# Kernel tuning notes

Measured on AMD Instinct MI355X. Metric: run time of the kernel, lower is better.

Reference implementation:

```python
import jax, jax.numpy as jnp
import numpy as np

D_MODEL = 128
D_STATE = 64
EXPAND = 2
D_INNER = EXPAND * D_MODEL  # 256
D_CONV = 4
DT_RANK = (D_MODEL + 15) // 16  # 8
EPS = 1e-6


def setup_inputs() -> dict:
    key = jax.random.key(0)
    ks = jax.random.split(key, 10)
    B, L = 8, 4096
    s = lambda *sh: 1.0 / np.sqrt(sh[-1])
    inp = {
        "x": jax.random.normal(ks[0], (B, L, D_MODEL), jnp.float32),
        "norm_w": jnp.ones((D_MODEL,), jnp.float32),
        "norm_b": jnp.zeros((D_MODEL,), jnp.float32),
        "in_proj_w": jax.random.normal(ks[1], (2 * D_INNER, D_MODEL), jnp.float32) * s(D_MODEL),
        "conv_w": jax.random.normal(ks[2], (D_INNER, 1, D_CONV), jnp.float32) * 0.5,
        "conv_b": jax.random.normal(ks[3], (D_INNER,), jnp.float32) * 0.02,
        "x_proj_w": jax.random.normal(ks[4], (DT_RANK + 2 * D_STATE, D_INNER), jnp.float32) * s(D_INNER),
        "dt_proj_w": jax.random.normal(ks[5], (D_INNER, DT_RANK), jnp.float32) * s(DT_RANK),
        "dt_proj_b": jax.random.uniform(ks[6], (D_INNER,), jnp.float32, -4.0, -2.0),  # softplus -> small dt
        "A_log": jnp.log(jnp.broadcast_to(jnp.arange(1.0, D_STATE + 1.0, dtype=jnp.float32), (D_INNER, D_STATE))),
        "D": jnp.ones((D_INNER,), jnp.float32),
        "out_proj_w": jax.random.normal(ks[7], (D_MODEL, D_INNER), jnp.float32) * s(D_INNER),
    }
    return inp


def _mamba_block(x, norm_w, norm_b, in_proj_w, conv_w, conv_b, x_proj_w,
                 dt_proj_w, dt_proj_b, A_log, Dp, out_proj_w):
    B, L, _ = x.shape
    # LayerNorm (eps=1e-6)
    mu = jnp.mean(x, -1, keepdims=True)
    var = jnp.mean(jnp.square(x - mu), -1, keepdims=True)
    h = (x - mu) * jax.lax.rsqrt(var + EPS) * norm_w + norm_b
    # in_proj -> (u, z), each (B, L, d_inner)
    xz = jnp.einsum('bld,ed->ble', h, in_proj_w)
    u, z = jnp.split(xz, 2, axis=-1)
    # causal depthwise conv1d over L, then SiLU
    u_nch = jnp.transpose(u, (0, 2, 1))  # (B, d_inner, L)
    u_conv = jax.lax.conv_general_dilated(
        u_nch, conv_w, window_strides=(1,), padding=[(D_CONV - 1, 0)],
        feature_group_count=D_INNER, dimension_numbers=('NCH', 'OIH', 'NCH'))
    u_conv = jax.nn.silu(u_conv + conv_b[None, :, None])
    u = jnp.transpose(u_conv, (0, 2, 1))  # (B, L, d_inner)
    # x_proj -> dt, Bmat, Cmat
    x_dbl = jnp.einsum('bld,ed->ble', u, x_proj_w)
    dt, Bmat, Cmat = jnp.split(x_dbl, [DT_RANK, DT_RANK + D_STATE], axis=-1)
    delta = jax.nn.softplus(jnp.einsum('blr,dr->bld', dt, dt_proj_w) + dt_proj_b)  # (B,L,d_inner)
    A = -jnp.exp(A_log)  # (d_inner, d_state)
    # selective scan over L: state (B, d_inner, d_state)
    def step(hS, inp):
        d_t, B_t, C_t, u_t = inp  # (B,dI),(B,N),(B,N),(B,dI)
        dA = jnp.exp(d_t[:, :, None] * A)                      # (B,dI,N)
        hS = dA * hS + (d_t * u_t)[:, :, None] * B_t[:, None, :]
        y = jnp.einsum('bdn,bn->bd', hS, C_t)
        return hS, y
    xs = (jnp.transpose(delta, (1, 0, 2)), jnp.transpose(Bmat, (1, 0, 2)),
          jnp.transpose(Cmat, (1, 0, 2)), jnp.transpose(u, (1, 0, 2)))
    h0 = jnp.zeros((B, D_INNER, D_STATE), x.dtype)
    _, ys = jax.lax.scan(step, h0, xs)
    y = jnp.transpose(ys, (1, 0, 2)) + u * Dp  # (B,L,d_inner)
    y = y * jax.nn.silu(z)
    out = jnp.einsum('bld,ed->ble', y, out_proj_w)  # (B,L,d_model)
    return x + out  # residual (drop_path=0)


def reference(x, norm_w, norm_b, in_proj_w, conv_w, conv_b, x_proj_w,
              dt_proj_w, dt_proj_b, A_log, D, out_proj_w):
    return _mamba_block(x, norm_w, norm_b, in_proj_w, conv_w, conv_b, x_proj_w,
                        dt_proj_w, dt_proj_b, A_log, D, out_proj_w)
```

## Files before the change

### kernel.cpp

```cpp
#include <hip/hip_runtime.h>
#include <math.h>

#define DM 128
#define DI 256
#define DSN 64
#define NB 8
#define LSEQ 4096
#define NTOK (NB*LSEQ)
#define GRP 8
#define GLEN (LSEQ/GRP)

typedef float4 f4;
typedef __attribute__((ext_vector_type(8))) short bf16x8;
typedef __attribute__((ext_vector_type(4))) float f32x4;
typedef __attribute__((ext_vector_type(8))) unsigned short us8;

#if __has_builtin(__builtin_amdgcn_exp2f)
#define EXP2(x) __builtin_amdgcn_exp2f(x)
#else
#define EXP2(x) __expf((x)*0.6931471805599453f)
#endif

__device__ __forceinline__ float sigmoidf_(float x){ return 1.f/(1.f+__expf(-x)); }
__device__ __forceinline__ float rdlane(float v, int j){
    return __int_as_float(__builtin_amdgcn_readlane(__float_as_int(v), j));
}
__device__ __forceinline__ unsigned short f2bf(float f){
    unsigned u = __float_as_uint(f);
    unsigned r = u + 0x7FFFu + ((u>>16)&1u);
    return (unsigned short)(r>>16);
}

__global__ void __launch_bounds__(256) k_lnstats(const float* __restrict__ x, float* __restrict__ stats){
    int tok = blockIdx.x*4 + (threadIdx.x>>6);
    int lane = threadIdx.x & 63;
    const float* row = x + (size_t)tok*DM;
    float a = row[lane], b = row[lane+64];
    float s = a+b, ss = a*a+b*b;
    #pragma unroll
    for (int off=32; off>0; off>>=1){ s += __shfl_xor(s,off); ss += __shfl_xor(ss,off); }
    if (lane==0){
        float mu = s*(1.f/128.f);
        float var = ss*(1.f/128.f) - mu*mu;
        stats[tok*2+0] = mu;
        stats[tok*2+1] = rsqrtf(var + 1e-6f);
    }
}

template<int N_DIM,int K_DIM,int MODE>
__global__ void __launch_bounds__(256) k_gemm_bf(const float* __restrict__ Af32,
    const unsigned short* __restrict__ Abf, const float* __restrict__ Bw,
    float* __restrict__ Cout, float* __restrict__ Cout2, int ldC,
    const float* __restrict__ stats, const float* __restrict__ nw,
    const float* __restrict__ nb, const float* __restrict__ resid)
{
    __shared__ unsigned short Abuf[128*72];
    __shared__ unsigned short Bbuf[64*72];
    const int tid = threadIdx.x;
    const int m0 = blockIdx.x*128;
    const int n0 = blockIdx.y*64;
    const int wave = tid>>6, lane = tid&63;
    const int wm = wave>>1, wn = wave&1;
    const int lr = lane&15, lk = (lane>>4)*8;
    f32x4 acc[4][2];
    #pragma unroll
    for (int i=0;i<4;++i){
        #pragma unroll
        for (int j=0;j<2;++j) acc[i][j] = (f32x4){0.f,0.f,0.f,0.f};
    }

    for (int k0=0; k0<K_DIM; k0+=64){
        {
            int row = tid>>1, ks = (tid&1)*32;
            int m = m0 + row;
            unsigned short* dst = &Abuf[row*72 + ks];
            if (MODE==2){
                const unsigned short* src = Abf + (size_t)m*K_DIM + k0 + ks;
                #pragma unroll
                for (int q=0;q<4;++q) *(us8*)(dst+q*8) = *(const us8*)(src+q*8);
            } else {
                const float* src = Af32 + (size_t)m*K_DIM + k0 + ks;
                float mu=0.f, rs=1.f;
                if (MODE==0){ mu = stats[2*m]; rs = stats[2*m+1]; }
                #pragma unroll
                for (int q=0;q<4;++q){
                    f4 v0 = *(const f4*)(src+q*8);
                    f4 v1 = *(const f4*)(src+q*8+4);
                    if (MODE==0){
                        int kk = k0+ks+q*8;
                        f4 w0=*(const f4*)(nw+kk), w1=*(const f4*)(nw+kk+4);
                        f4 c0=*(const f4*)(nb+kk), c1=*(const f4*)(nb+kk+4);
                        v0.x=(v0.x-mu)*rs*w0.x+c0.x; v0.y=(v0.y-mu)*rs*w0.y+c0.y;
                        v0.z=(v0.z-mu)*rs*w0.z+c0.z; v0.w=(v0.w-mu)*rs*w0.w+c0.w;
                        v1.x=(v1.x-mu)*rs*w1.x+c1.x; v1.y=(v1.y-mu)*rs*w1.y+c1.y;
                        v1.z=(v1.z-mu)*rs*w1.z+c1.z; v1.w=(v1.w-mu)*rs*w1.w+c1.w;
                    }
                    us8 o = {f2bf(v0.x),f2bf(v0.y),f2bf(v0.z),f2bf(v0.w),
                             f2bf(v1.x),f2bf(v1.y),f2bf(v1.z),f2bf(v1.w)};
                    *(us8*)(dst+q*8) = o;
                }
            }
        }
        {
            int row = tid>>2, ks = (tid&3)*16;
            int n = n0 + row;
            unsigned short* dst = &Bbuf[row*72 + ks];
            #pragma unroll
            for (int q=0;q<2;++q){
                f4 v0={0.f,0.f,0.f,0.f}, v1={0.f,0.f,0.f,0.f};
                if (N_DIM%64==0 || n < N_DIM){
                    const float* src = Bw + (size_t)n*K_DIM + k0 + ks + q*8;
                    v0 = *(const f4*)src; v1 = *(const f4*)(src+4);
                }
                us8 o = {f2bf(v0.x),f2bf(v0.y),f2bf(v0.z),f2bf(v0.w),
                         f2bf(v1.x),f2bf(v1.y),f2bf(v1.z),f2bf(v1.w)};
                *(us8*)(dst+q*8) = o;
            }
        }
        __syncthreads();
        #pragma unroll
        for (int kk=0; kk<64; kk+=32){
            bf16x8 bfr[2], afr[4];
            #pragma unroll
            for (int fn=0;fn<2;++fn)
                bfr[fn] = *(const bf16x8*)&Bbuf[(wn*32+fn*16+lr)*72 + kk + lk];
            #pragma unroll
            for (int fm=0;fm<4;++fm)
                afr[fm] = *(const bf16x8*)&Abuf[(wm*64+fm*16+lr)*72 + kk + lk];
            #pragma unroll
            for (int fm=0;fm<4;++fm){
                #pragma unroll
                for (int fn=0;fn<2;++fn)
                    acc[fm][fn] = __builtin_amdgcn_mfma_f32_16x16x32_bf16(afr[fm], bfr[fn], acc[fm][fn], 0,0,0);
            }
        }
        __syncthreads();
    }
    const int cb = (lane>>4)*4;
    #pragma unroll
    for (int fm=0;fm<4;++fm){
        #pragma unroll
        for (int fn=0;fn<2;++fn){
            int col = n0 + wn*32 + fn*16 + lr;
            if (N_DIM%64!=0 && col >= N_DIM) continue;
            #pragma unroll
            for (int r=0;r<4;++r){
                int m = m0 + wm*64 + fm*16 + cb + r;
                float v = acc[fm][fn][r];
                if (MODE==1){
                    if (col < 8) Cout2[(size_t)m*8 + col] = v;
                    else         Cout[(size_t)m*128 + (col-8)] = v;
                } else {
                    if (MODE==2) v += resid[(size_t)m*N_DIM + col];
                    Cout[(size_t)m*ldC + col] = v;
                }
            }
        }
    }
}

__global__ void __launch_bounds__(256) k_trans(const float* __restrict__ ygT,
    const float* __restrict__ xz, unsigned short* __restrict__ ygbf)
{
    __shared__ float T[64][65];
    int t0 = blockIdx.x*64;
    int w  = blockIdx.y;
    int b  = w>>2, d0 = (w&3)*64;
    int tid = threadIdx.x;
    {
        int dl = tid>>2, ts = (tid&3)*16;
        const float* src = ygT + ((size_t)(b*DI + d0 + dl))*LSEQ + t0 + ts;
        #pragma unroll
        for (int q=0;q<4;++q) *(f4*)&T[dl][ts+q*4] = *(const f4*)(src+q*4);
    }
    __syncthreads();
    {
        int tl = tid>>2, ds8 = (tid&3)*16;
        size_t tok = (size_t)(b*LSEQ + t0 + tl);
        const float* zsrc = xz + tok*(2*DI) + DI + d0 + ds8;
        unsigned short* dst = ygbf + tok*DI + d0 + ds8;
        f4 z0 = *(const f4*)zsrc,      z1 = *(const f4*)(zsrc+4);
        f4 z2 = *(const f4*)(zsrc+8),  z3 = *(const f4*)(zsrc+12);
        float zz[16] = {z0.x,z0.y,z0.z,z0.w, z1.x,z1.y,z1.z,z1.w,
                        z2.x,z2.y,z2.z,z2.w, z3.x,z3.y,z3.z,z3.w};
        us8 o0, o1;
        #pragma unroll
        for (int j=0;j<8;++j){
            float g0 = zz[j]   * sigmoidf_(zz[j]);
            float g1 = zz[j+8] * sigmoidf_(zz[j+8]);
            o0[j] = f2bf(T[ds8+j][tl]   * g0);
            o1[j] = f2bf(T[ds8+8+j][tl] * g1);
        }
        *(us8*)dst = o0; *(us8*)(dst+8) = o1;
    }
}

__global__ void __launch_bounds__(256) k_conv(const float* __restrict__ xz,
    const float* __restrict__ cw, const float* __restrict__ cb, float* __restrict__ u)
{
    int idx = blockIdx.x*256 + threadIdx.x;
    int dq = idx & 63;
    int tok = idx >> 6;
    int t = tok & (LSEQ-1);
    f4 w0 = *(const f4*)(cw + (dq*4+0)*4);
    f4 w1 = *(const f4*)(cw + (dq*4+1)*4);
    f4 w2 = *(const f4*)(cw + (dq*4+2)*4);
    f4 w3 = *(const f4*)(cw + (dq*4+3)*4);
    f4 r  = *(const f4*)(cb + dq*4);
    #pragma unroll
    for (int j=0;j<4;++j){
        int tj = t-3+j;
        if (tj < 0) continue;
        f4 v = *(const f4*)(xz + (size_t)(tok-3+j)*(2*DI) + dq*4);
        r.x = fmaf(v.x, ((const float*)&w0)[j], r.x);
        r.y = fmaf(v.y, ((const float*)&w1)[j], r.y);
        r.z = fmaf(v.z, ((const float*)&w2)[j], r.z);
        r.w = fmaf(v.w, ((const float*)&w3)[j], r.w);
    }
    r.x *= sigmoidf_(r.x); r.y *= sigmoidf_(r.y);
    r.z *= sigmoidf_(r.z); r.w *= sigmoidf_(r.w);
    *(f4*)(u + (size_t)tok*DI + dq*4) = r;
}

__global__ void __launch_bounds__(256) k_delta(const float* __restrict__ dt_c,
    const float* __restrict__ Wdt, const float* __restrict__ bdt, float* __restrict__ delta)
{
    int d = threadIdx.x;
    int tok0 = blockIdx.x * 16;
    f4 w0 = *(const f4*)(Wdt + d*8);
    f4 w1 = *(const f4*)(Wdt + d*8 + 4);
    float bias = bdt[d];
    __shared__ float dts[16][8];
    if (threadIdx.x < 128){
        int ti = threadIdx.x >> 3, r = threadIdx.x & 7;
        dts[ti][r] = dt_c[(size_t)(tok0+ti)*8 + r];
    }
    __syncthreads();
    #pragma unroll 4
    for (int ti=0; ti<16; ++ti){
        f4 d0 = *(const f4*)&dts[ti][0];
        f4 d1 = *(const f4*)&dts[ti][4];
        float v = bias;
        v = fmaf(d0.x,w0.x, v); v = fmaf(d0.y,w0.y, v);
        v = fmaf(d0.z,w0.z, v); v = fmaf(d0.w,w0.w, v);
        v = fmaf(d1.x,w1.x, v); v = fmaf(d1.y,w1.y, v);
        v = fmaf(d1.z,w1.z, v); v = fmaf(d1.w,w1.w, v);
        float sp = (v > 20.f) ? v : log1pf(__expf(v));
        delta[(size_t)(tok0+ti)*DI + d] = sp;
    }
}

__global__ void __launch_bounds__(256,8) k_scan1(const float* __restrict__ delta,
    const float* __restrict__ u, const float* __restrict__ bc,
    const float* __restrict__ alog, float* __restrict__ hfin, float* __restrict__ aprod)
{
    int bid = blockIdx.x;
    int b = bid & 7;
    int i = bid >> 3;
    int g = i % 7;
    int dblk = i / 7;
    int wave = threadIdx.x >> 6, lane = threadIdx.x & 63;
    int d = dblk*4 + wave;
    int tok0 = b*LSEQ + g*GLEN;
    const float* dptr = delta + (size_t)tok0*DI + d;
    const float* uptr = u     + (size_t)tok0*DI + d;
    float Acoef = -__expf(alog[d*DSN + lane]) * 1.44269504f;
    float h = 0.f, cum = 0.f;
    float Bpf[8];
    {
        const float* bp = bc + (size_t)tok0*128 + lane;
        #pragma unroll
        for (int k8=0;k8<8;++k8) Bpf[k8] = bp[k8*128];
    }
    const float* bpn = bc + (size_t)(tok0+8)*128 + lane;

    for (int c=0;c<GLEN/64;++c){
        float dv = dptr[(size_t)(c*64+lane)*DI];
        float uv = uptr[(size_t)(c*64+lane)*DI];
        float duv = dv*uv;
        float cs = dv;
        #pragma unroll
        for (int off=32; off; off>>=1) cs += __shfl_xor(cs, off);
        cum += cs;
        #pragma unroll 1
        for (int g8=0;g8<8;++g8){
            #pragma unroll
            for (int k8=0;k8<8;++k8){
                int j = g8*8 + k8;
                float Bn = Bpf[k8];
                Bpf[k8] = bpn[k8*128];
                float sd  = rdlane(dv,  j);
                float sdu = rdlane(duv, j);
                float a = EXP2(Acoef*sd);
                h = fmaf(a, h, sdu*Bn);
            }
            bpn += 8*128;
        }
    }
    size_t idx = ((size_t)(b*DI + d)*GRP + g)*DSN + lane;
    hfin[idx]  = h;
    aprod[idx] = EXP2(Acoef*cum);
}

__global__ void __launch_bounds__(256) k_comb(const float* __restrict__ hfin,
    const float* __restrict__ aprod, float* __restrict__ hin)
{
    int bd = blockIdx.x*4 + (threadIdx.x>>6);
    int lane = threadIdx.x & 63;
    size_t base = (size_t)bd*GRP*DSN + lane;
    float h = 0.f;
    hin[base] = 0.f;
    #pragma unroll
    for (int g=0; g<GRP-1; ++g){
        float hf = hfin[base + (size_t)g*DSN];
        float ap = aprod[base + (size_t)g*DSN];
        h = fmaf(ap, h, hf);
        hin[base + (size_t)(g+1)*DSN] = h;
    }
}

__global__ void __launch_bounds__(256,7) k_scan2(const float* __restrict__ delta,
    const float* __restrict__ u, const float* __restrict__ bc,
    const float* __restrict__ alog, const float* __restrict__ Dp,
    const float* __restrict__ hin, float* __restrict__ ygT)
{
    __shared__ float Q[4][64][17];
    int bid = blockIdx.x;
    int b = bid & 7;
    int i = bid >> 3;
    int g = i & 7;
    int dblk = i >> 3;
    int wave = threadIdx.x >> 6, lane = threadIdx.x & 63;
    int d = dblk*4 + wave;
    int bd = b*DI + d;
    int tok0 = b*LSEQ + g*GLEN;
    float Acoef = -__expf(alog[d*DSN + lane]) * 1.44269504f;
    float Dd = Dp[d];
    float h = hin[((size_t)bd*GRP + g)*DSN + lane];
    const float* dptr = delta + (size_t)tok0*DI + d;
    const float* uptr = u     + (size_t)tok0*DI + d;
    float* yout = ygT + (size_t)bd*LSEQ + g*GLEN;
    float (*Qw)[17] = Q[wave];
    int q16 = (lane>>4)*16;
    int cidx = lane & 15;
    float Bpf[8], Cpf[8];
    {
        const float* bp = bc + (size_t)tok0*128 + lane;
        #pragma unroll
        for (int k8=0;k8<8;++k8){ Bpf[k8] = bp[k8*128]; Cpf[k8] = bp[k8*128 + 64]; }
    }
    const float* bpn = bc + (size_t)(tok0+8)*128 + lane;

    for (int c=0;c<GLEN/64;++c){
        float dv = dptr[(size_t)(c*64+lane)*DI];
        float uv = uptr[(size_t)(c*64+lane)*DI];
        float duv = dv*uv;
        float y = 0.f;
        #pragma unroll 1
        for (int m2=0;m2<4;++m2){
            #pragma unroll 1
            for (int half=0; half<2; ++half){
                #pragma unroll
                for (int k8=0;k8<8;++k8){
                    int j = m2*16 + half*8 + k8;
                    float Bn = Bpf[k8], Cn = Cpf[k8];
                    Bpf[k8] = bpn[k8*128];
                    Cpf[k8] = bpn[k8*128 + 64];
                    float sd  = rdlane(dv,  j);
                    float sdu = rdlane(duv, j);
                    float a = EXP2(Acoef*sd);
                    h = fmaf(a, h, sdu*Bn);
                    Qw[lane][half*8+k8] = h*Cn;
                }
                bpn += 8*128;
            }
            float r = 0.f;
            #pragma unroll
            for (int ii=0;ii<16;++ii) r += Qw[q16+ii][cidx];
            r += __shfl_xor(r, 16);
            r += __shfl_xor(r, 32);
            y = ((lane>>4)==m2) ? r : y;
        }
        yout[c*64 + lane] = fmaf(uv, Dd, y);
    }
}

extern "C" void kernel_launch(void* const* d_in, const int* in_sizes, int n_in,
                              void* d_out, int out_size, void* d_ws, size_t ws_size,
                              hipStream_t stream)
{
    (void)in_sizes; (void)n_in; (void)out_size; (void)ws_size;
    const float* x    = (const float*)d_in[0];
    const float* nw   = (const float*)d_in[1];
    const float* nb   = (const float*)d_in[2];
    const float* w_in = (const float*)d_in[3];
    const float* cw   = (const float*)d_in[4];
    const float* cb   = (const float*)d_in[5];
    const float* wx   = (const float*)d_in[6];
    const float* wdt  = (const float*)d_in[7];
    const float* bdt  = (const float*)d_in[8];
    const float* alog = (const float*)d_in[9];
    const float* Dp   = (const float*)d_in[10];
    const float* wo   = (const float*)d_in[11];
    float* out = (float*)d_out;

    float* ws    = (float*)d_ws;
    float* xz    = ws;
    float* u     = xz    + (size_t)NTOK*2*DI;
    float* bcp   = u     + (size_t)NTOK*DI;
    float* dt_c  = bcp   + (size_t)NTOK*128 + 2048;
    float* delta = dt_c  + (size_t)NTOK*8;
    float* ygT   = delta + (size_t)NTOK*DI;
    float* stats = ygT   + (size_t)NTOK*DI;
    float* hfin  = stats + (size_t)NTOK*2;
    float* aprod = hfin  + (size_t)NB*DI*GRP*DSN;
    float* hin   = aprod + (size_t)NB*DI*GRP*DSN;
    unsigned short* ygbf = (unsigned short*)(hin + (size_t)NB*DI*GRP*DSN);

    k_lnstats<<<NTOK/4, 256, 0, stream>>>(x, stats);

    dim3 g1(NTOK/128, 512/64);
    k_gemm_bf<512,128,0><<<g1, 256, 0, stream>>>(x, nullptr, w_in, xz, nullptr, 512, stats, nw, nb, nullptr);

    k_conv<<<NTOK*64/256, 256, 0, stream>>>(xz, cw, cb, u);

    dim3 g2(NTOK/128, 3);
    k_gemm_bf<136,256,1><<<g2, 256, 0, stream>>>(u, nullptr, wx, bcp, dt_c, 0, nullptr, nullptr, nullptr, nullptr);

    k_delta<<<NTOK/16, 256, 0, stream>>>(dt_c, wdt, bdt, delta);

    k_scan1<<<NB*(GRP-1)*64, 256, 0, stream>>>(delta, u, bcp, alog, hfin, aprod);
    k_comb<<<NB*DI/4, 256, 0, stream>>>(hfin, aprod, hin);
    k_scan2<<<NB*GRP*64, 256, 0, stream>>>(delta, u, bcp, alog, Dp, hin, ygT);

    dim3 gt(LSEQ/64, NB*4);
    k_trans<<<gt, 256, 0, stream>>>(ygT, xz, ygbf);

    dim3 g3(NTOK/128, 2);
    k_gemm_bf<128,256,2><<<g3, 256, 0, stream>>>(nullptr, ygbf, wo, out, nullptr, 128, nullptr, nullptr, nullptr, x);
}
```

Baseline: 484.7 us.

## Store delta and delta*u transposed and interleaved for contiguous scan loads

Replaces the delta kernel with one that computes softplus delta and delta*u together and writes them interleaved in a channel-major (b,d,t) layout through a shared-memory transpose. Both scan kernels then read one contiguous float2 per lane instead of two strided loads across the token dimension. The D*u skip term moves from scan2 into the transpose/gating kernel, which now also reads u. The intermediate buffer doubles in size and k_trans does extra loads.

```diff
diff --git a/kernel.cpp b/kernel.cpp
--- a/kernel.cpp
+++ b/kernel.cpp
@@ -160,7 +160,8 @@
 }
 
 __global__ void __launch_bounds__(256) k_trans(const float* __restrict__ ygT,
-    const float* __restrict__ xz, unsigned short* __restrict__ ygbf)
+    const float* __restrict__ xz, const float* __restrict__ u,
+    const float* __restrict__ Dp, unsigned short* __restrict__ ygbf)
 {
     __shared__ float T[64][65];
     int t0 = blockIdx.x*64;
@@ -178,18 +179,32 @@
         int tl = tid>>2, ds8 = (tid&3)*16;
         size_t tok = (size_t)(b*LSEQ + t0 + tl);
         const float* zsrc = xz + tok*(2*DI) + DI + d0 + ds8;
+        const float* usrc = u  + tok*DI + d0 + ds8;
         unsigned short* dst = ygbf + tok*DI + d0 + ds8;
         f4 z0 = *(const f4*)zsrc,      z1 = *(const f4*)(zsrc+4);
         f4 z2 = *(const f4*)(zsrc+8),  z3 = *(const f4*)(zsrc+12);
+        f4 u0 = *(const f4*)usrc,      u1 = *(const f4*)(usrc+4);
+        f4 u2 = *(const f4*)(usrc+8),  u3 = *(const f4*)(usrc+12);
+        f4 D0 = *(const f4*)(Dp+d0+ds8),   f4_1;
+        f4 D1 = *(const f4*)(Dp+d0+ds8+4);
+        f4 D2 = *(const f4*)(Dp+d0+ds8+8);
+        f4 D3 = *(const f4*)(Dp+d0+ds8+12);
+        (void)f4_1;
         float zz[16] = {z0.x,z0.y,z0.z,z0.w, z1.x,z1.y,z1.z,z1.w,
                         z2.x,z2.y,z2.z,z2.w, z3.x,z3.y,z3.z,z3.w};
+        float uu[16] = {u0.x,u0.y,u0.z,u0.w, u1.x,u1.y,u1.z,u1.w,
+                        u2.x,u2.y,u2.z,u2.w, u3.x,u3.y,u3.z,u3.w};
+        float DD[16] = {D0.x,D0.y,D0.z,D0.w, D1.x,D1.y,D1.z,D1.w,
+                        D2.x,D2.y,D2.z,D2.w, D3.x,D3.y,D3.z,D3.w};
         us8 o0, o1;
         #pragma unroll
         for (int j=0;j<8;++j){
             float g0 = zz[j]   * sigmoidf_(zz[j]);
             float g1 = zz[j+8] * sigmoidf_(zz[j+8]);
-            o0[j] = f2bf(T[ds8+j][tl]   * g0);
-            o1[j] = f2bf(T[ds8+8+j][tl] * g1);
+            float y0 = fmaf(DD[j],   uu[j],   T[ds8+j][tl]);
+            float y1 = fmaf(DD[j+8], uu[j+8], T[ds8+8+j][tl]);
+            o0[j] = f2bf(y0 * g0);
+            o1[j] = f2bf(y1 * g1);
         }
         *(us8*)dst = o0; *(us8*)(dst+8) = o1;
     }
@@ -222,37 +237,63 @@
     *(f4*)(u + (size_t)tok*DI + dq*4) = r;
 }
 
-__global__ void __launch_bounds__(256) k_delta(const float* __restrict__ dt_c,
-    const float* __restrict__ Wdt, const float* __restrict__ bdt, float* __restrict__ delta)
-{
-    int d = threadIdx.x;
-    int tok0 = blockIdx.x * 16;
+__global__ void __launch_bounds__(256) k_ddt(const float* __restrict__ dt_c,
+    const float* __restrict__ u, const float* __restrict__ Wdt,
+    const float* __restrict__ bdt, float* __restrict__ ddT)
+{
+    __shared__ float dts[64][8];
+    __shared__ float2 T2[64][65];
+    int t0 = blockIdx.x*64;
+    int w  = blockIdx.y;
+    int b  = w>>2, d0 = (w&3)*64;
+    int tid = threadIdx.x;
+    {
+        int ti = tid>>2, r2 = (tid&3)*2;
+        const float* src = dt_c + (size_t)(b*LSEQ + t0 + ti)*8 + r2;
+        dts[ti][r2] = src[0]; dts[ti][r2+1] = src[1];
+    }
+    int dl = tid & 63;
+    int d  = d0 + dl;
+    int tof = tid >> 6;
     f4 w0 = *(const f4*)(Wdt + d*8);
     f4 w1 = *(const f4*)(Wdt + d*8 + 4);
     float bias = bdt[d];
-    __shared__ float dts[16][8];
-    if (threadIdx.x < 128){
-        int ti = threadIdx.x >> 3, r = threadIdx.x & 7;
-        dts[ti][r] = dt_c[(size_t)(tok0+ti)*8 + r];
-    }
     __syncthreads();
     #pragma unroll 4
-    for (int ti=0; ti<16; ++ti){
-        f4 d0 = *(const f4*)&dts[ti][0];
-        f4 d1 = *(const f4*)&dts[ti][4];
+    for (int tq=0; tq<16; ++tq){
+        int t = tq*4 + tof;
+        float uv = u[(size_t)(b*LSEQ + t0 + t)*DI + d];
+        f4 a0 = *(const f4*)&dts[t][0];
+        f4 a1 = *(const f4*)&dts[t][4];
         float v = bias;
-        v = fmaf(d0.x,w0.x, v); v = fmaf(d0.y,w0.y, v);
-        v = fmaf(d0.z,w0.z, v); v = fmaf(d0.w,w0.w, v);
-        v = fmaf(d1.x,w1.x, v); v = fmaf(d1.y,w1.y, v);
-        v = fmaf(d1.z,w1.z, v); v = fmaf(d1.w,w1.w, v);
+        v = fmaf(a0.x,w0.x,v); v = fmaf(a0.y,w0.y,v);
+        v = fmaf(a0.z,w0.z,v); v = fmaf(a0.w,w0.w,v);
+        v = fmaf(a1.x,w1.x,v); v = fmaf(a1.y,w1.y,v);
+        v = fmaf(a1.w,w1.w,fmaf(a1.z,w1.z,0.f)) + v;
         float sp = (v > 20.f) ? v : log1pf(__expf(v));
-        delta[(size_t)(tok0+ti)*DI + d] = sp;
-    }
-}
-
-__global__ void __launch_bounds__(256,8) k_scan1(const float* __restrict__ delta,
-    const float* __restrict__ u, const float* __restrict__ bc,
-    const float* __restrict__ alog, float* __restrict__ hfin, float* __restrict__ aprod)
+        T2[dl][t] = (float2){sp, sp*uv};
+    }
+    __syncthreads();
+    {
+        int row = tid>>2, seg = (tid&3)*16;
+        float* dst = ddT + ((size_t)(b*DI + d0 + row)*LSEQ + t0 + seg)*2;
+        #pragma unroll
+        for (int k=0;k<4;++k){
+            float2 a0 = T2[row][seg+k*4+0];
+            float2 a1 = T2[row][seg+k*4+1];
+            float2 a2 = T2[row][seg+k*4+2];
+            float2 a3 = T2[row][seg+k*4+3];
+            f4 o0 = {a0.x,a0.y,a1.x,a1.y};
+            f4 o1 = {a2.x,a2.y,a3.x,a3.y};
+            *(f4*)(dst + k*8)     = o0;
+            *(f4*)(dst + k*8 + 4) = o1;
+        }
+    }
+}
+
+__global__ void __launch_bounds__(256,8) k_scan1(const float* __restrict__ ddT,
+    const float* __restrict__ bc, const float* __restrict__ alog,
+    float* __restrict__ hfin, float* __restrict__ aprod)
 {
     int bid = blockIdx.x;
     int b = bid & 7;
@@ -262,8 +303,7 @@
     int wave = threadIdx.x >> 6, lane = threadIdx.x & 63;
     int d = dblk*4 + wave;
     int tok0 = b*LSEQ + g*GLEN;
-    const float* dptr = delta + (size_t)tok0*DI + d;
-    const float* uptr = u     + (size_t)tok0*DI + d;
+    const float* ddp = ddT + ((size_t)(b*DI + d)*LSEQ + g*GLEN)*2;
     float Acoef = -__expf(alog[d*DSN + lane]) * 1.44269504f;
     float h = 0.f, cum = 0.f;
     float Bpf[8];
@@ -275,9 +315,8 @@
     const float* bpn = bc + (size_t)(tok0+8)*128 + lane;
 
     for (int c=0;c<GLEN/64;++c){
-        float dv = dptr[(size_t)(c*64+lane)*DI];
-        float uv = uptr[(size_t)(c*64+lane)*DI];
-        float duv = dv*uv;
+        float2 dd = *(const float2*)&ddp[(c*64+lane)*2];
+        float dv = dd.x, duv = dd.y;
         float cs = dv;
         #pragma unroll
         for (int off=32; off; off>>=1) cs += __shfl_xor(cs, off);
@@ -319,9 +358,8 @@
     }
 }
 
-__global__ void __launch_bounds__(256,7) k_scan2(const float* __restrict__ delta,
-    const float* __restrict__ u, const float* __restrict__ bc,
-    const float* __restrict__ alog, const float* __restrict__ Dp,
+__global__ void __launch_bounds__(256,7) k_scan2(const float* __restrict__ ddT,
+    const float* __restrict__ bc, const float* __restrict__ alog,
     const float* __restrict__ hin, float* __restrict__ ygT)
 {
     __shared__ float Q[4][64][17];
@@ -335,10 +373,8 @@
     int bd = b*DI + d;
     int tok0 = b*LSEQ + g*GLEN;
     float Acoef = -__expf(alog[d*DSN + lane]) * 1.44269504f;
-    float Dd = Dp[d];
     float h = hin[((size_t)bd*GRP + g)*DSN + lane];
-    const float* dptr = delta + (size_t)tok0*DI + d;
-    const float* uptr = u     + (size_t)tok0*DI + d;
+    const float* ddp = ddT + ((size_t)bd*LSEQ + g*GLEN)*2;
     float* yout = ygT + (size_t)bd*LSEQ + g*GLEN;
     float (*Qw)[17] = Q[wave];
     int q16 = (lane>>4)*16;
@@ -352,9 +388,8 @@
     const float* bpn = bc + (size_t)(tok0+8)*128 + lane;
 
     for (int c=0;c<GLEN/64;++c){
-        float dv = dptr[(size_t)(c*64+lane)*DI];
-        float uv = uptr[(size_t)(c*64+lane)*DI];
-        float duv = dv*uv;
+        float2 dd = *(const float2*)&ddp[(c*64+lane)*2];
+        float dv = dd.x, duv = dd.y;
         float y = 0.f;
         #pragma unroll 1
         for (int m2=0;m2<4;++m2){
@@ -381,7 +416,7 @@
             r += __shfl_xor(r, 32);
             y = ((lane>>4)==m2) ? r : y;
         }
-        yout[c*64 + lane] = fmaf(uv, Dd, y);
+        yout[c*64 + lane] = y;
     }
 }
 
@@ -409,8 +444,8 @@
     float* u     = xz    + (size_t)NTOK*2*DI;
     float* bcp   = u     + (size_t)NTOK*DI;
     float* dt_c  = bcp   + (size_t)NTOK*128 + 2048;
-    float* delta = dt_c  + (size_t)NTOK*8;
-    float* ygT   = delta + (size_t)NTOK*DI;
+    float* ddT   = dt_c  + (size_t)NTOK*8;
+    float* ygT   = ddT   + (size_t)NTOK*512;
     float* stats = ygT   + (size_t)NTOK*DI;
     float* hfin  = stats + (size_t)NTOK*2;
     float* aprod = hfin  + (size_t)NB*DI*GRP*DSN;
@@ -427,14 +462,15 @@
     dim3 g2(NTOK/128, 3);
     k_gemm_bf<136,256,1><<<g2, 256, 0, stream>>>(u, nullptr, wx, bcp, dt_c, 0, nullptr, nullptr, nullptr, nullptr);
 
-    k_delta<<<NTOK/16, 256, 0, stream>>>(dt_c, wdt, bdt, delta);
-
-    k_scan1<<<NB*(GRP-1)*64, 256, 0, stream>>>(delta, u, bcp, alog, hfin, aprod);
+    dim3 gd(LSEQ/64, NB*4);
+    k_ddt<<<gd, 256, 0, stream>>>(dt_c, u, wdt, bdt, ddT);
+
+    k_scan1<<<NB*(GRP-1)*64, 256, 0, stream>>>(ddT, bcp, alog, hfin, aprod);
     k_comb<<<NB*DI/4, 256, 0, stream>>>(hfin, aprod, hin);
-    k_scan2<<<NB*GRP*64, 256, 0, stream>>>(delta, u, bcp, alog, Dp, hin, ygT);
+    k_scan2<<<NB*GRP*64, 256, 0, stream>>>(ddT, bcp, alog, hin, ygT);
 
     dim3 gt(LSEQ/64, NB*4);
-    k_trans<<<gt, 256, 0, stream>>>(ygT, xz, ygbf);
+    k_trans<<<gt, 256, 0, stream>>>(ygT, xz, u, Dp, ygbf);
 
     dim3 g3(NTOK/128, 2);
     k_gemm_bf<128,256,2><<<g3, 256, 0, stream>>>(nullptr, ygbf, wo, out, nullptr, 128, nullptr, nullptr, nullptr, x);
```

New measurement: 501.7 us. +3.5%, slower.
